# Kernel tuning notes

Hardware: AMD Instinct MI355X
Metric: run time of the kernel (lower is better)

## Reference

```python
import jax, jax.numpy as jnp
import numpy as np

NUM_ELMT = 64
INPUT_DIM = 16
BOUND = 50.0
MESH_RATIO = 1.2
N_POINTS = 1_048_576


def _build_mesh():
    m = NUM_ELMT
    one_step = BOUND * (MESH_RATIO - 1.0) / (MESH_RATIO ** (m / 2) - 1.0)
    idx = np.arange(-m / 2, m / 2 + 1)
    mesh = (MESH_RATIO ** np.abs(idx) - 1.0) / (MESH_RATIO - 1.0) * one_step * np.sign(idx)
    mesh_norm = (mesh + BOUND) / (2.0 * BOUND)
    mesh_norm = np.concatenate([[0.0], mesh_norm[1:-1], [1.0]]).astype(np.float32)
    elmt_size = (mesh_norm[1:] - mesh_norm[:-1]).astype(np.float32)
    return jnp.asarray(mesh_norm), jnp.asarray(elmt_size)


def setup_inputs() -> dict:
    key = jax.random.key(0)
    k1, k2 = jax.random.split(key)
    x = jax.random.uniform(k1, (N_POINTS, INPUT_DIM), jnp.float32, minval=-BOUND, maxval=BOUND)
    pdj = jnp.ones((N_POINTS, 1), jnp.float32)
    sldj = jnp.zeros((N_POINTS, 1), jnp.float32)
    log_p = 0.1 * jax.random.normal(k2, (NUM_ELMT - 1, INPUT_DIM), jnp.float32)
    mesh_norm, elmt_size = _build_mesh()
    return {"x": x, "pdj": pdj, "sldj": sldj, "log_p": log_p,
            "mesh_norm": mesh_norm, "elmt_size": elmt_size}


def _normalize_pdf(log_p, elmt_size):
    # elmt_size: (M,) -> (M,1) column, log_p: (M-1, D)
    es = elmt_size[:, None]
    ep = jnp.exp(log_p)
    px = ep * (es[:-1] + es[1:]) / 2.0
    px = ep * (1.0 - es[0]) / jnp.sum(px, axis=0, keepdims=True)
    p0 = jnp.ones((1, log_p.shape[1]), log_p.dtype)
    pdf_norm = jnp.concatenate([p0, px, p0], axis=0)            # (M+1, D)
    cell = (pdf_norm[:-1] + pdf_norm[1:]) / 2.0 * es            # (M, D)
    # F_ref[i] = sum(cell[:i]); single cumsum instead of the O(M^2) torch loop
    F_ref = jnp.concatenate([jnp.zeros_like(p0), jnp.cumsum(cell, axis=0)[:-1]], axis=0)  # (M, D)
    return pdf_norm, F_ref


def reference(x, pdj, sldj, log_p, mesh_norm, elmt_size):
    pdf_norm, F_ref = _normalize_pdf(log_p, elmt_size)
    xn = (x + BOUND) / (2.0 * BOUND)                            # (N, D) in [0,1]
    k = jnp.searchsorted(mesh_norm, xn, side='left')            # (N, D), torch right=False
    cover = (k != 0) & (k != NUM_ELMT + 1)
    k = jnp.clip(k, 1, NUM_ELMT)
    km1 = k - 1
    v1 = jnp.take_along_axis(pdf_norm, km1, axis=0)             # pdf at lower node
    v2 = jnp.take_along_axis(pdf_norm, k, axis=0)               # pdf at upper node
    xmodi = xn - mesh_norm[km1]                                 # offset inside element
    h = elmt_size[km1]                                          # element width
    F_pre = jnp.take_along_axis(F_ref, km1, axis=0)             # CDF at lower node
    y = jnp.where(cover, F_pre + xmodi * xmodi * 0.5 * (v2 - v1) / h + xmodi * v1, xn)
    abs_det = jnp.where(cover, xmodi * (v2 - v1) / h + v1, 1.0)
    pdj_out = pdj * jnp.prod(abs_det, axis=-1, keepdims=True)
    sldj_out = sldj + jnp.sum(jnp.log(abs_det), axis=-1, keepdims=True)
    x_out = y * 2.0 * BOUND - BOUND
    return (x_out, pdj_out, sldj_out)
```

## Files before the change

kernel.cpp:

```cpp
#include <hip/hip_runtime.h>
#include <math.h>


namespace {
constexpr int DIM = 16;
constexpr int ME  = 64;
constexpr float BOUNDF = 50.0f;
constexpr float K1      = 6.8164378f;
constexpr float INV_L2R = 3.8017840f;
constexpr int COEF_FLOATS = ME * 68;
constexpr int EP_BASE     = COEF_FLOATS - 63 * DIM;
}

__global__ __launch_bounds__(256) void nll_kernel(
    const float* __restrict__ x,
    const float* __restrict__ pdj,
    const float* __restrict__ sldj,
    const float* __restrict__ log_p,
    const float* __restrict__ mesh_norm,
    float* __restrict__ out,
    int npts)
{
  __shared__ __align__(16) float co[COEF_FLOATS];
  __shared__ float s_mesh[ME + 1];

  const int tid = threadIdx.x;

  if (tid <= ME) s_mesh[tid] = mesh_norm[tid];
  for (int i = tid; i < 63 * DIM; i += 256)
    co[EP_BASE + i] = __expf(log_p[i]);
  __syncthreads();

  const int wv = tid >> 6, lane = tid & 63;
  float epv[4];
#pragma unroll
  for (int i = 0; i < 4; ++i)
    epv[i] = (lane < 63) ? co[EP_BASE + lane * DIM + (4 * wv + i)] : 0.f;
  const float mj  = s_mesh[lane];
  const float mj1 = s_mesh[lane + 1];
  const float mj2 = s_mesh[(lane + 2 > ME) ? ME : (lane + 2)];
  const float es0 = s_mesh[1] - s_mesh[0];
  __syncthreads();

  const float h = mj1 - mj;
#pragma unroll
  for (int i = 0; i < 4; ++i) {
    const int d = 4 * wv + i;
    const float ep = epv[i];
    float ss = (lane < 63) ? ep * (mj2 - mj) : 0.f;
    ss += __shfl_xor(ss, 1);  ss += __shfl_xor(ss, 2);  ss += __shfl_xor(ss, 4);
    ss += __shfl_xor(ss, 8);  ss += __shfl_xor(ss, 16); ss += __shfl_xor(ss, 32);
    const float scale = (1.0f - es0) / (0.5f * ss);
    const float cur = (lane < 63) ? ep * scale : 1.0f;
    float prev = __shfl_up(cur, 1);
    if (lane == 0) prev = 1.0f;
    const float cell = (prev + cur) * 0.5f * h;
    float v = cell, o;
    o = __shfl_up(v, 1);  if (lane >= 1)  v += o;
    o = __shfl_up(v, 2);  if (lane >= 2)  v += o;
    o = __shfl_up(v, 4);  if (lane >= 4)  v += o;
    o = __shfl_up(v, 8);  if (lane >= 8)  v += o;
    o = __shfl_up(v, 16); if (lane >= 16) v += o;
    o = __shfl_up(v, 32); if (lane >= 32) v += o;
    const float F = v - cell;
    const float A = 0.5f * (cur - prev) / h;
    const float B = fmaf(-(A + A), mj, prev);
    const float D = fmaf(mj, fmaf(mj, A, -prev), F);
    *reinterpret_cast<float4*>(&co[lane * 68 + 4 * d]) = make_float4(A, B, D, A + A);
  }
  __syncthreads();

  const int stride = gridDim.x * blockDim.x;
  const float4* __restrict__ x4 = reinterpret_cast<const float4*>(x);
  float4* __restrict__ out4 = reinterpret_cast<float4*>(out);
  const int np16 = npts * DIM;

  for (int p = blockIdx.x * blockDim.x + tid; p < npts; p += stride) {
    float4 X[4];
#pragma unroll
    for (int q = 0; q < 4; ++q) X[q] = x4[4 * p + q];
    const float* vals = reinterpret_cast<const float*>(X);
    float yv[16];
    float prod = 1.f;

#pragma unroll
    for (int j = 0; j < 16; ++j) {
      const float val = vals[j];
      const float xn = (val + BOUNDF) * 0.01f;
      const float u = fmaf(fabsf(val), K1, 1.0f);
      const float n = __log2f(u) * INV_L2R;
      const int k32 = (int)ceilf(copysignf(n, val));
      int km1 = k32 + 31;
      km1 = km1 < 0 ? 0 : (km1 > 63 ? 63 : km1);
      const float4 cf = *reinterpret_cast<const float4*>(&co[km1 * 68 + 4 * j]);
      float y  = fmaf(xn, fmaf(xn, cf.x, cf.y), cf.z);
      float dt = fmaf(xn, cf.w, cf.y);
      const bool cover = (xn > 0.f) && (xn <= 1.0f);
      y  = cover ? y  : xn;
      dt = cover ? dt : 1.0f;
      yv[j] = fmaf(y, 2.0f * BOUNDF, -BOUNDF);
      prod *= dt;
    }

    float4* o4 = &out4[4 * p];
#pragma unroll
    for (int q = 0; q < 4; ++q)
      o4[q] = make_float4(yv[4 * q], yv[4 * q + 1], yv[4 * q + 2], yv[4 * q + 3]);
    out[np16 + p]        = pdj[p] * prod;
    out[np16 + npts + p] = sldj[p] + __logf(prod);
  }
}

extern "C" void kernel_launch(void* const* d_in, const int* in_sizes, int n_in,
                              void* d_out, int out_size, void* d_ws, size_t ws_size,
                              hipStream_t stream) {
  const float* x    = (const float*)d_in[0];
  const float* pdj  = (const float*)d_in[1];
  const float* sldj = (const float*)d_in[2];
  const float* lp   = (const float*)d_in[3];
  const float* mesh = (const float*)d_in[4];
  float* out = (float*)d_out;

  const int npts  = in_sizes[0] / DIM;
  const int block = 256;
  int grid = 2048;
  const int needed = (npts + block - 1) / block;
  if (needed < grid) grid = needed;

  hipLaunchKernelGGL(nll_kernel, dim3(grid), dim3(block), 0, stream,
                     x, pdj, sldj, lp, mesh, out, npts);
}
```

Before: 37.51 us.

## Split each point across two lanes, combine product via shuffle

Each point's 16 dimensions are now split across two adjacent threads, with eight dimensions each. The two partial determinant products are combined with a lane shuffle, and one thread writes pdj while the other writes sldj. This doubles the thread-level parallelism and halves the per-thread register footprint. It also batches the LDS coefficient loads ahead of the math to improve latency hiding. In exchange, each point needs an extra shuffle, and the loop relies on pairs staying in lockstep, which requires an even total count.

```diff
diff --git a/kernel.cpp b/kernel.cpp
--- a/kernel.cpp
+++ b/kernel.cpp
@@ -19,7 +19,7 @@
     const float* __restrict__ log_p,
     const float* __restrict__ mesh_norm,
     float* __restrict__ out,
-    int npts)
+    int npts, int npairs)
 {
   __shared__ __align__(16) float co[COEF_FLOATS];
   __shared__ float s_mesh[ME + 1];
@@ -70,44 +70,58 @@
   }
   __syncthreads();
 
-  const int stride = gridDim.x * blockDim.x;
+  const int tpg = gridDim.x * blockDim.x;
   const float4* __restrict__ x4 = reinterpret_cast<const float4*>(x);
   float4* __restrict__ out4 = reinterpret_cast<float4*>(out);
   const int np16 = npts * DIM;
 
-  for (int p = blockIdx.x * blockDim.x + tid; p < npts; p += stride) {
-    float4 X[4];
+  for (int t = blockIdx.x * blockDim.x + tid; t < npairs; t += tpg) {
+    const int p  = t >> 1;
+    const int hh = t & 1;
+    const float4 xa = x4[2 * t];
+    const float4 xb = x4[2 * t + 1];
+    const float ps = hh ? sldj[p] : pdj[p];
+    const float vals[8] = {xa.x, xa.y, xa.z, xa.w, xb.x, xb.y, xb.z, xb.w};
+
+    float xn[8];
+    int   off[8];
 #pragma unroll
-    for (int q = 0; q < 4; ++q) X[q] = x4[4 * p + q];
-    const float* vals = reinterpret_cast<const float*>(X);
-    float yv[16];
-    float prod = 1.f;
-
-#pragma unroll
-    for (int j = 0; j < 16; ++j) {
+    for (int j = 0; j < 8; ++j) {
       const float val = vals[j];
-      const float xn = (val + BOUNDF) * 0.01f;
+      xn[j] = (val + BOUNDF) * 0.01f;
       const float u = fmaf(fabsf(val), K1, 1.0f);
       const float n = __log2f(u) * INV_L2R;
-      const int k32 = (int)ceilf(copysignf(n, val));
-      int km1 = k32 + 31;
+      int km1 = 31 + (int)ceilf(copysignf(n, val));
       km1 = km1 < 0 ? 0 : (km1 > 63 ? 63 : km1);
-      const float4 cf = *reinterpret_cast<const float4*>(&co[km1 * 68 + 4 * j]);
-      float y  = fmaf(xn, fmaf(xn, cf.x, cf.y), cf.z);
-      float dt = fmaf(xn, cf.w, cf.y);
-      const bool cover = (xn > 0.f) && (xn <= 1.0f);
-      y  = cover ? y  : xn;
-      dt = cover ? dt : 1.0f;
-      yv[j] = fmaf(y, 2.0f * BOUNDF, -BOUNDF);
-      prod *= dt;
+      off[j] = km1 * 68 + (((hh << 3) + j) << 2);
     }
 
-    float4* o4 = &out4[4 * p];
+    float4 cf[8];
 #pragma unroll
-    for (int q = 0; q < 4; ++q)
-      o4[q] = make_float4(yv[4 * q], yv[4 * q + 1], yv[4 * q + 2], yv[4 * q + 3]);
-    out[np16 + p]        = pdj[p] * prod;
-    out[np16 + npts + p] = sldj[p] + __logf(prod);
+    for (int j = 0; j < 8; ++j)
+      cf[j] = *reinterpret_cast<const float4*>(&co[off[j]]);
+
+    float yv[8], dt[8];
+#pragma unroll
+    for (int j = 0; j < 8; ++j) {
+      const float z = xn[j];
+      float y = fmaf(z, fmaf(z, cf[j].x, cf[j].y), cf[j].z);
+      float d = fmaf(z, cf[j].w, cf[j].y);
+      const bool cover = (z > 0.f) && (z <= 1.0f);
+      y = cover ? y : z;
+      d = cover ? d : 1.0f;
+      yv[j] = fmaf(y, 2.0f * BOUNDF, -BOUNDF);
+      dt[j] = d;
+    }
+    const float prod = ((dt[0] * dt[1]) * (dt[2] * dt[3])) *
+                       ((dt[4] * dt[5]) * (dt[6] * dt[7]));
+
+    out4[2 * t]     = make_float4(yv[0], yv[1], yv[2], yv[3]);
+    out4[2 * t + 1] = make_float4(yv[4], yv[5], yv[6], yv[7]);
+
+    const float full = prod * __shfl_xor(prod, 1);
+    const float res  = hh ? (ps + __logf(full)) : (ps * full);
+    out[np16 + hh * npts + p] = res;
   }
 }
 
@@ -121,12 +135,13 @@
   const float* mesh = (const float*)d_in[4];
   float* out = (float*)d_out;
 
-  const int npts  = in_sizes[0] / DIM;
-  const int block = 256;
+  const int npts   = in_sizes[0] / DIM;
+  const int npairs = npts * 2;
+  const int block  = 256;
   int grid = 2048;
-  const int needed = (npts + block - 1) / block;
+  const int needed = (npairs + block - 1) / block;
   if (needed < grid) grid = needed;
 
   hipLaunchKernelGGL(nll_kernel, dim3(grid), dim3(block), 0, stream,
-                     x, pdj, sldj, lp, mesh, out, npts);
+                     x, pdj, sldj, lp, mesh, out, npts, npairs);
 }
```

Result: faster. 33.94 us (-9.5%).

## Software-pipeline global loads, batch LDS reads via inline asm, use nontemporal stores

Applied to the files above, without the earlier changes.

Restructures the grid-stride loop so the next point's x, pdj and sldj are loaded before the current point is computed, overlapping global memory latency with work. All 16 coefficient LDS reads are issued up front with inline ds_read_b128, and partial lgkmcnt waits let the first half be computed while the second half is still in flight. Outputs are written with nontemporal stores to reduce cache pollution, and the product uses a tree reduction to shorten the dependency chain. The cost is higher register pressure and hand-written asm waitcnts that bypass the compiler's scheduling.

```diff
diff --git a/kernel.cpp b/kernel.cpp
--- a/kernel.cpp
+++ b/kernel.cpp
@@ -1,5 +1,6 @@
 #include <hip/hip_runtime.h>
 #include <math.h>
+#include <stdint.h>
 
 
 namespace {
@@ -10,6 +11,13 @@
 constexpr float INV_L2R = 3.8017840f;
 constexpr int COEF_FLOATS = ME * 68;
 constexpr int EP_BASE     = COEF_FLOATS - 63 * DIM;
+}
+
+typedef float f32x4 __attribute__((ext_vector_type(4)));
+
+__device__ __forceinline__ void nt_store4(float* p, float a, float b, float c, float d) {
+  f32x4 v = {a, b, c, d};
+  __builtin_nontemporal_store(v, reinterpret_cast<f32x4*>(p));
 }
 
 __global__ __launch_bounds__(256) void nll_kernel(
@@ -70,44 +78,111 @@
   }
   __syncthreads();
 
-  const int stride = gridDim.x * blockDim.x;
+  const int tpg = gridDim.x * blockDim.x;
   const float4* __restrict__ x4 = reinterpret_cast<const float4*>(x);
-  float4* __restrict__ out4 = reinterpret_cast<float4*>(out);
   const int np16 = npts * DIM;
-
-  for (int p = blockIdx.x * blockDim.x + tid; p < npts; p += stride) {
-    float4 X[4];
-#pragma unroll
-    for (int q = 0; q < 4; ++q) X[q] = x4[4 * p + q];
-    const float* vals = reinterpret_cast<const float*>(X);
-    float yv[16];
-    float prod = 1.f;
-
+  const uint32_t lds_base = (uint32_t)(uintptr_t)(&co[0]);
+
+  int p = blockIdx.x * blockDim.x + tid;
+  if (p >= npts) return;
+
+  float4 X0 = x4[4 * p + 0], X1 = x4[4 * p + 1], X2 = x4[4 * p + 2], X3 = x4[4 * p + 3];
+  float pv = pdj[p], sv = sldj[p];
+
+  while (true) {
+    const int pn = p + tpg;
+    const bool more = pn < npts;
+
+    float4 XN0, XN1, XN2, XN3;
+    float pvn = 0.f, svn = 0.f;
+    if (more) {
+      XN0 = x4[4 * pn + 0]; XN1 = x4[4 * pn + 1];
+      XN2 = x4[4 * pn + 2]; XN3 = x4[4 * pn + 3];
+      pvn = pdj[pn]; svn = sldj[pn];
+    }
+
+    float vals[16];
+    *reinterpret_cast<float4*>(&vals[0])  = X0;
+    *reinterpret_cast<float4*>(&vals[4])  = X1;
+    *reinterpret_cast<float4*>(&vals[8])  = X2;
+    *reinterpret_cast<float4*>(&vals[12]) = X3;
+
+    float xn[16];
+    uint32_t adr[16];
 #pragma unroll
     for (int j = 0; j < 16; ++j) {
       const float val = vals[j];
-      const float xn = (val + BOUNDF) * 0.01f;
+      xn[j] = (val + BOUNDF) * 0.01f;
       const float u = fmaf(fabsf(val), K1, 1.0f);
       const float n = __log2f(u) * INV_L2R;
-      const int k32 = (int)ceilf(copysignf(n, val));
-      int km1 = k32 + 31;
+      int km1 = 31 + (int)ceilf(copysignf(n, val));
       km1 = km1 < 0 ? 0 : (km1 > 63 ? 63 : km1);
-      const float4 cf = *reinterpret_cast<const float4*>(&co[km1 * 68 + 4 * j]);
-      float y  = fmaf(xn, fmaf(xn, cf.x, cf.y), cf.z);
-      float dt = fmaf(xn, cf.w, cf.y);
-      const bool cover = (xn > 0.f) && (xn <= 1.0f);
-      y  = cover ? y  : xn;
-      dt = cover ? dt : 1.0f;
-      yv[j] = fmaf(y, 2.0f * BOUNDF, -BOUNDF);
-      prod *= dt;
-    }
-
-    float4* o4 = &out4[4 * p];
-#pragma unroll
-    for (int q = 0; q < 4; ++q)
-      o4[q] = make_float4(yv[4 * q], yv[4 * q + 1], yv[4 * q + 2], yv[4 * q + 3]);
-    out[np16 + p]        = pdj[p] * prod;
-    out[np16 + npts + p] = sldj[p] + __logf(prod);
+      adr[j] = lds_base + (uint32_t)((km1 * 68 + (j << 2)) << 2);
+    }
+
+    float4 c0, c1, c2, c3, c4, c5, c6, c7, c8, c9, cA, cB, cC, cD, cE, cF;
+    asm volatile("ds_read_b128 %0, %1" : "=v"(c0) : "v"(adr[0]));
+    asm volatile("ds_read_b128 %0, %1" : "=v"(c1) : "v"(adr[1]));
+    asm volatile("ds_read_b128 %0, %1" : "=v"(c2) : "v"(adr[2]));
+    asm volatile("ds_read_b128 %0, %1" : "=v"(c3) : "v"(adr[3]));
+    asm volatile("ds_read_b128 %0, %1" : "=v"(c4) : "v"(adr[4]));
+    asm volatile("ds_read_b128 %0, %1" : "=v"(c5) : "v"(adr[5]));
+    asm volatile("ds_read_b128 %0, %1" : "=v"(c6) : "v"(adr[6]));
+    asm volatile("ds_read_b128 %0, %1" : "=v"(c7) : "v"(adr[7]));
+    asm volatile("ds_read_b128 %0, %1" : "=v"(c8) : "v"(adr[8]));
+    asm volatile("ds_read_b128 %0, %1" : "=v"(c9) : "v"(adr[9]));
+    asm volatile("ds_read_b128 %0, %1" : "=v"(cA) : "v"(adr[10]));
+    asm volatile("ds_read_b128 %0, %1" : "=v"(cB) : "v"(adr[11]));
+    asm volatile("ds_read_b128 %0, %1" : "=v"(cC) : "v"(adr[12]));
+    asm volatile("ds_read_b128 %0, %1" : "=v"(cD) : "v"(adr[13]));
+    asm volatile("ds_read_b128 %0, %1" : "=v"(cE) : "v"(adr[14]));
+    asm volatile("ds_read_b128 %0, %1" : "=v"(cF) : "v"(adr[15]));
+
+    float yv[16], dt[16];
+    asm volatile("s_waitcnt lgkmcnt(8)" ::: "memory");
+    __builtin_amdgcn_sched_barrier(0);
+    {
+      const float4 cfh[8] = {c0, c1, c2, c3, c4, c5, c6, c7};
+#pragma unroll
+      for (int j = 0; j < 8; ++j) {
+        const float z = xn[j];
+        float y = fmaf(z, fmaf(z, cfh[j].x, cfh[j].y), cfh[j].z);
+        float d = fmaf(z, cfh[j].w, cfh[j].y);
+        const bool cover = (z > 0.f) && (z <= 1.0f);
+        yv[j] = fmaf(cover ? y : z, 2.0f * BOUNDF, -BOUNDF);
+        dt[j] = cover ? d : 1.0f;
+      }
+    }
+    asm volatile("s_waitcnt lgkmcnt(0)" ::: "memory");
+    __builtin_amdgcn_sched_barrier(0);
+    {
+      const float4 cfh[8] = {c8, c9, cA, cB, cC, cD, cE, cF};
+#pragma unroll
+      for (int j = 0; j < 8; ++j) {
+        const float z = xn[8 + j];
+        float y = fmaf(z, fmaf(z, cfh[j].x, cfh[j].y), cfh[j].z);
+        float d = fmaf(z, cfh[j].w, cfh[j].y);
+        const bool cover = (z > 0.f) && (z <= 1.0f);
+        yv[8 + j] = fmaf(cover ? y : z, 2.0f * BOUNDF, -BOUNDF);
+        dt[8 + j] = cover ? d : 1.0f;
+      }
+    }
+
+    const float prod = (((dt[0] * dt[1]) * (dt[2] * dt[3])) *
+                        ((dt[4] * dt[5]) * (dt[6] * dt[7]))) *
+                       (((dt[8] * dt[9]) * (dt[10] * dt[11])) *
+                        ((dt[12] * dt[13]) * (dt[14] * dt[15])));
+
+    float* ob = out + 16 * p;
+    nt_store4(ob + 0,  yv[0],  yv[1],  yv[2],  yv[3]);
+    nt_store4(ob + 4,  yv[4],  yv[5],  yv[6],  yv[7]);
+    nt_store4(ob + 8,  yv[8],  yv[9],  yv[10], yv[11]);
+    nt_store4(ob + 12, yv[12], yv[13], yv[14], yv[15]);
+    __builtin_nontemporal_store(pv * prod, out + np16 + p);
+    __builtin_nontemporal_store(sv + __logf(prod), out + np16 + npts + p);
+
+    if (!more) break;
+    p = pn; X0 = XN0; X1 = XN1; X2 = XN2; X3 = XN3; pv = pvn; sv = svn;
   }
 }
 
```

New measurement: 81.65 us. 118% more time.
